# Kernel optimization log

Hardware: AMD Instinct MI355X
Metric: run time of the kernel (lower is better)

## Reference

```python
import jax, jax.numpy as jnp
import numpy as np

SEQ, B, E, H, V = 70, 128, 512, 1024, 10000


def setup_inputs() -> dict:
    key = jax.random.key(0)
    ks = jax.random.split(key, 24)
    u = lambda k, sh, a: jax.random.uniform(k, sh, jnp.float32, -a, a)
    kh = float(1.0 / np.sqrt(H))
    inp = {
        "inputs": jax.random.randint(ks[0], (SEQ, B), 0, V, dtype=jnp.int32),
        "hidden": jnp.zeros((2, B, H), jnp.float32),
        "emb_W": u(ks[1], (V, E), 0.1),
        "out_W": u(ks[2], (V, H), 0.1),
        "out_b": jnp.zeros((V,), jnp.float32),
    }
    i = 3
    for l, in_sz in enumerate([E, H]):
        for name, sh in [("Wir", (H, in_sz)), ("Wiz", (H, in_sz)), ("Wih", (H, in_sz)),
                         ("Whr", (H, H)), ("Whz", (H, H)), ("Whh", (H, H))]:
            inp[f"l{l}_{name}"] = u(ks[i], sh, kh); i += 1
        for name in ["bir", "biz", "bih"]:
            inp[f"l{l}_{name}"] = u(ks[i], (H,), kh); i += 1
    return inp


def gru_layer(xs, h0, Wir, bir, Whr, Wiz, biz, Whz, Wih, bih, Whh):
    # Precompute input-side projections for the whole sequence (big fused gemms).
    xr = jnp.einsum('sbe,he->sbh', xs, Wir) + bir  # (S,B,H)
    xz = jnp.einsum('sbe,he->sbh', xs, Wiz) + biz
    xh = jnp.einsum('sbe,he->sbh', xs, Wih) + bih

    def step(h, x_t):
        xr_t, xz_t, xh_t = x_t
        r = jax.nn.sigmoid(xr_t + h @ Whr.T)
        z = jax.nn.sigmoid(xz_t + h @ Whz.T)
        h1 = jnp.tanh(xh_t + r * (h @ Whh.T))
        h_new = (1.0 - z) * h1 + z * h
        return h_new, h_new

    hT, ys = jax.lax.scan(step, h0, (xr, xz, xh))
    return ys, hT


def reference(inputs, hidden, emb_W, out_W, out_b,
              l0_Wir, l0_Wiz, l0_Wih, l0_Whr, l0_Whz, l0_Whh, l0_bir, l0_biz, l0_bih,
              l1_Wir, l1_Wiz, l1_Wih, l1_Whr, l1_Whz, l1_Whh, l1_bir, l1_biz, l1_bih):
    emb = emb_W[inputs]  # (S,B,E)
    ys0, h0T = gru_layer(emb, hidden[0], l0_Wir, l0_bir, l0_Whr,
                         l0_Wiz, l0_biz, l0_Whz, l0_Wih, l0_bih, l0_Whh)
    ys1, h1T = gru_layer(ys0, hidden[1], l1_Wir, l1_bir, l1_Whr,
                         l1_Wiz, l1_biz, l1_Whz, l1_Wih, l1_bih, l1_Whh)
    logits = jnp.einsum('sbh,vh->sbv', ys1, out_W) + out_b  # (S,B,V)
    return logits, jnp.stack([h0T, h1T])
```

## Files before the change

kernel.cpp:

```cpp
#include <hip/hip_runtime.h>
#include <hip/hip_bf16.h>

#define SEQn 70
#define Bn 128
#define En 512
#define Hn 1024
#define Vn 10000
#define VPADn 10240
#define Mn (SEQn*Bn)
#define H3n (3*Hn)
#define BHn (Bn*Hn)
#define NBLK 192

typedef __hip_bfloat16 bf16;
typedef __attribute__((ext_vector_type(8))) short short8;
typedef __attribute__((ext_vector_type(4))) float f32x4;

__device__ __forceinline__ bf16 f2bf(float x){ return __float2bfloat16(x); }
__device__ __forceinline__ float bf2f(bf16 x){ return __bfloat162float(x); }

__device__ __forceinline__ void gl_lds16(const void* g, void* l){
  __builtin_amdgcn_global_load_lds((const __attribute__((address_space(1))) unsigned int*)g,
                                   (__attribute__((address_space(3))) unsigned int*)l, 16, 0, 0);
}


__global__ void cat3_w(const float* __restrict__ a, const float* __restrict__ b,
                       const float* __restrict__ c, bf16* __restrict__ d, int n){
  int i = blockIdx.x * 256 + threadIdx.x;
  if (i >= 3*n) return;
  const float* s = (i < n) ? a : ((i < 2*n) ? b : c);
  int off = (i < n) ? i : ((i < 2*n) ? i - n : i - 2*n);
  d[i] = f2bf(s[off]);
}

__global__ void cat3_f(const float* __restrict__ a, const float* __restrict__ b,
                       const float* __restrict__ c, float* __restrict__ d, int n){
  int i = blockIdx.x * 256 + threadIdx.x;
  if (i >= 3*n) return;
  d[i] = (i < n) ? a[i] : ((i < 2*n) ? b[i - n] : c[i - 2*n]);
}

__global__ void f2b_k(const float* __restrict__ s, bf16* __restrict__ d, int n){
  int i = blockIdx.x * 256 + threadIdx.x;
  if (i < n) d[i] = f2bf(s[i]);
}

__global__ void conv_outw(const float* __restrict__ s, bf16* __restrict__ d){
  long i = (long)blockIdx.x * 256 + threadIdx.x;
  if (i >= (long)VPADn * Hn) return;
  int row = (int)(i >> 10);
  d[i] = (row < Vn) ? f2bf(s[i]) : f2bf(0.f);
}

__global__ void embed_k(const int* __restrict__ idx, const float* __restrict__ eW,
                        bf16* __restrict__ out){
  const int sb = blockIdx.x;
  const int t = idx[sb];
  const float* s = eW + (long)t * En;
  bf16* d = out + (long)sb * En;
  for (int e = threadIdx.x; e < En; e += 256) d[e] = f2bf(s[e]);
}


template<bool OB, bool NB>
__global__ __launch_bounds__(256)
void gemm_bt(const bf16* __restrict__ A, const bf16* __restrict__ Bm,
             const float* __restrict__ bias, void* __restrict__ C,
             int K, int ldc, int nvalid)
{
  __shared__ __align__(16) bf16 As[128*64];
  __shared__ __align__(16) bf16 Bs[128*64];
  const int tid = threadIdx.x;
  const int l = tid & 63, w = tid >> 6;
  const int lr = l & 15, lk = l >> 4;
  const int wm = (w >> 1) * 64, wn = (w & 1) * 64;
  const int mt = blockIdx.y, nt = blockIdx.x;
  const bf16* Ag = A + (long)mt * 128 * K;
  const bf16* Bg = Bm + (long)nt * 128 * K;

  f32x4 acc[4][4] = {};

  for (int kb = 0; kb < K; kb += 64) {
#pragma unroll
    for (int r = 0; r < 4; ++r) {
      const int u = r * 256 + tid;
      const int row = u >> 3, kus = (u & 7) ^ (row & 7);
      gl_lds16(Ag + (long)row * K + kb + kus * 8, (char*)As + (r * 256 + w * 64) * 16);
    }
#pragma unroll
    for (int r = 0; r < 4; ++r) {
      const int u = r * 256 + tid;
      const int row = u >> 3, kus = (u & 7) ^ (row & 7);
      gl_lds16(Bg + (long)row * K + kb + kus * 8, (char*)Bs + (r * 256 + w * 64) * 16);
    }
    __syncthreads();
#pragma unroll
    for (int kh = 0; kh < 2; ++kh) {
      const int ku = kh * 4 + lk;
      short8 af[4], bfv[4];
#pragma unroll
      for (int i = 0; i < 4; ++i) {
        const int ar = wm + i * 16 + lr;
        af[i]  = *(const short8*)((const char*)As + ar * 128 + ((ku ^ (ar & 7)) * 16));
        const int br = wn + i * 16 + lr;
        bfv[i] = *(const short8*)((const char*)Bs + br * 128 + ((ku ^ (br & 7)) * 16));
      }
#pragma unroll
      for (int i = 0; i < 4; ++i)
#pragma unroll
        for (int j = 0; j < 4; ++j)
          acc[i][j] = __builtin_amdgcn_mfma_f32_16x16x32_bf16(af[i], bfv[j], acc[i][j], 0, 0, 0);
    }
    __syncthreads();
  }

#pragma unroll
  for (int i = 0; i < 4; ++i) {
#pragma unroll
    for (int j = 0; j < 4; ++j) {
      const int col = nt * 128 + wn + j * 16 + lr;
      const bool cok = (!NB) || (col < nvalid);
      const float bv = cok ? bias[col] : 0.f;
      const int row = mt * 128 + wm + i * 16 + lk * 4;
      if (cok) {
#pragma unroll
        for (int r = 0; r < 4; ++r) {
          const float v = acc[i][j][r] + bv;
          if (OB) ((bf16*)C)[(long)(row + r) * ldc + col] = f2bf(v);
          else    ((float*)C)[(long)(row + r) * ldc + col] = v;
        }
      }
    }
  }
}


#define LOADQ(buf, base)                                                     \
  _Pragma("unroll")                                                          \
  for (int q = 0; q < 8; ++q)                                                \
    buf[q] = *(const short8*)(Arow + ((base) + q) * 32 + lk * 8);

#define MFMAQ(buf, base)                                                     \
  _Pragma("unroll")                                                          \
  for (int q = 0; q < 8; ++q) {                                              \
    _Pragma("unroll")                                                        \
    for (int g = 0; g < 3; ++g) {                                            \
      const int brow = g * 16 + lr;                                          \
      const short8 bfrag = *(const short8*)(smem +                           \
          (size_t)(brow * 128 + ((((base) + q) * 4 + lk) ^ (brow & 7))) * 16); \
      acc[g] = __builtin_amdgcn_mfma_f32_16x16x32_bf16(buf[q], bfrag, acc[g], 0, 0, 0); \
    }                                                                        \
  }

__global__ __launch_bounds__(512, 2)
void gru_persist(const bf16* __restrict__ Wh0, const bf16* __restrict__ Wi1,
                 const bf16* __restrict__ Wh1, const float* __restrict__ b1,
                 const float* __restrict__ hidden, bf16* __restrict__ xg,
                 bf16* __restrict__ ys0, bf16* __restrict__ ys1,
                 float* __restrict__ hT, unsigned* __restrict__ bar)
{
  __shared__ __align__(16) char smem[98304];

  const int tid = threadIdx.x;
  const int lane = tid & 63, wid = tid >> 6;
  const int wbase = tid & ~63;
  const int lr = lane & 15, lk = lane >> 4;
  const int role = blockIdx.x >> 6, nb = blockIdx.x & 63;
  const int col0 = nb * 16;
  const int col = col0 + lr;

  unsigned myxcd;
  asm("s_getreg_b32 %0, hwreg(20, 0, 32)" : "=s"(myxcd));
  myxcd &= 7;
  unsigned* larrp  = bar + myxcd * 64;
  unsigned* gbarp  = bar + 512;
  unsigned* gflagp = bar + 544;

  const bf16* Wsrc = (role == 0) ? Wh0 : ((role == 1) ? Wi1 : Wh1);
#pragma unroll
  for (int it = 0; it < 12; ++it) {
    const int L = it * 512 + tid;
    const int row = L >> 7, up = L & 127, u = up ^ (row & 7);
    const int g3 = row >> 4, rr = row & 15;
    gl_lds16(Wsrc + ((size_t)(g3 * Hn + col0 + rr)) * Hn + (size_t)u * 8,
             smem + (it * 512 + wbase) * 16);
  }

  f32x4 hreg = {};
  float bv[3] = {};
  if (role != 1) {
    const float* hsrc = hidden + (role == 2 ? BHn : 0);
#pragma unroll
    for (int r = 0; r < 4; ++r)
      hreg[r] = hsrc[(size_t)(wid * 16 + lk * 4 + r) * Hn + col];
  } else {
#pragma unroll
    for (int g = 0; g < 3; ++g) bv[g] = b1[g * Hn + col];
  }
  asm volatile("s_waitcnt vmcnt(0)" ::: "memory");
  __syncthreads();

  unsigned perxcd = 0;
  if (tid == 0) {
    (void)__hip_atomic_fetch_add(larrp, 1u, __ATOMIC_RELAXED, __HIP_MEMORY_SCOPE_WORKGROUP);
    asm volatile("s_waitcnt vmcnt(0)" ::: "memory");
    unsigned g = __hip_atomic_fetch_add(gbarp, 1u, __ATOMIC_RELAXED, __HIP_MEMORY_SCOPE_AGENT);
    if (g == NBLK - 1)
      __hip_atomic_store(gflagp, 1u, __ATOMIC_RELAXED, __HIP_MEMORY_SCOPE_AGENT);
    while (__hip_atomic_load(gflagp, __ATOMIC_RELAXED, __HIP_MEMORY_SCOPE_AGENT) < 1u)
      __builtin_amdgcn_s_sleep(2);
    perxcd = __hip_atomic_fetch_add(larrp, 0u, __ATOMIC_RELAXED, __HIP_MEMORY_SCOPE_WORKGROUP);
  }
  __syncthreads();

  const int arow = wid * 16 + lr;

  for (int s = 0; s < 72; ++s) {
    const int t = s - role;
    if (t >= 0 && t < SEQn) {
      const bf16* Asrc = (role == 0) ? (ys0 + (size_t)t * BHn)
                       : (role == 1) ? (ys0 + (size_t)(t + 1) * BHn)
                                     : (ys1 + (size_t)t * BHn);
      const bf16* Arow = Asrc + (size_t)arow * Hn;
      f32x4 acc[3] = {};
      short8 aA[8], aB[8];
      unsigned short xus[12];
      LOADQ(aA, 0)
      LOADQ(aB, 8)
      if (role != 1) {
        const bf16* xsrc = xg + (size_t)t * Bn * (size_t)H3n;
#pragma unroll
        for (int g = 0; g < 3; ++g)
#pragma unroll
          for (int r = 0; r < 4; ++r) {
            const int row = wid * 16 + lk * 4 + r;
            const unsigned short* p =
                (const unsigned short*)(xsrc + (size_t)row * H3n + g * Hn + col);
            xus[g * 4 + r] = (role == 2)
              ? __hip_atomic_load((unsigned short*)p, __ATOMIC_RELAXED, __HIP_MEMORY_SCOPE_AGENT)
              : *p;
          }
      }
      MFMAQ(aA, 0)
      LOADQ(aA, 16)
      MFMAQ(aB, 8)
      LOADQ(aB, 24)
      MFMAQ(aA, 16)
      MFMAQ(aB, 24)

      if (role == 1) {
#pragma unroll
        for (int g = 0; g < 3; ++g)
#pragma unroll
          for (int r = 0; r < 4; ++r) {
            const int row = wid * 16 + lk * 4 + r;
            unsigned short v = __builtin_bit_cast(unsigned short, f2bf(acc[g][r] + bv[g]));
            __hip_atomic_store(
                (unsigned short*)&xg[((size_t)t * Bn + row) * H3n + g * Hn + col],
                v, __ATOMIC_RELAXED, __HIP_MEMORY_SCOPE_AGENT);
          }
      } else {
        bf16* ydst = ((role == 0) ? ys0 : ys1) + (size_t)(t + 1) * BHn;
#pragma unroll
        for (int r = 0; r < 4; ++r) {
          const int row = wid * 16 + lk * 4 + r;
          const float xr = bf2f(__builtin_bit_cast(bf16, xus[r]));
          const float xz = bf2f(__builtin_bit_cast(bf16, xus[4 + r]));
          const float xh = bf2f(__builtin_bit_cast(bf16, xus[8 + r]));
          const float rg = 1.f / (1.f + __expf(-(xr + acc[0][r])));
          const float zg = 1.f / (1.f + __expf(-(xz + acc[1][r])));
          const float hc = tanhf(xh + rg * acc[2][r]);
          const float hn = (1.f - zg) * hc + zg * hreg[r];
          hreg[r] = hn;
          unsigned short v = __builtin_bit_cast(unsigned short, f2bf(hn));
          __hip_atomic_store((unsigned short*)&ydst[(size_t)row * Hn + col],
                             v, __ATOMIC_RELAXED, __HIP_MEMORY_SCOPE_AGENT);
          if (t == SEQn - 1)
            hT[(role == 0 ? 0 : BHn) + (size_t)row * Hn + col] = hn;
        }
      }
    }
    if (s < 71) {
      __syncthreads();
      if (tid == 0) {
        unsigned a = __hip_atomic_fetch_add(larrp, 1u, __ATOMIC_RELAXED,
                                            __HIP_MEMORY_SCOPE_WORKGROUP);
        if (a == perxcd * (unsigned)(s + 2) - 1u) {
          unsigned g = __hip_atomic_fetch_add(gbarp, perxcd, __ATOMIC_RELAXED,
                                              __HIP_MEMORY_SCOPE_AGENT);
          if (g + perxcd == (unsigned)NBLK * (unsigned)(s + 2))
            __hip_atomic_store(gflagp, (unsigned)(s + 2), __ATOMIC_RELAXED,
                               __HIP_MEMORY_SCOPE_AGENT);
        }
        while (__hip_atomic_load(gflagp, __ATOMIC_RELAXED,
                                 __HIP_MEMORY_SCOPE_AGENT) < (unsigned)(s + 2))
          __builtin_amdgcn_s_sleep(2);
      }
      __syncthreads();
    }
  }
}


extern "C" void kernel_launch(void* const* d_in, const int* in_sizes, int n_in,
                              void* d_out, int out_size, void* d_ws, size_t ws_size,
                              hipStream_t stream)
{
  (void)in_sizes; (void)n_in; (void)out_size; (void)ws_size;
  const int*   inp    = (const int*)d_in[0];
  const float* hidden = (const float*)d_in[1];
  const float* embW   = (const float*)d_in[2];
  const float* outW   = (const float*)d_in[3];
  const float* outb   = (const float*)d_in[4];

  char* p = (char*)d_ws;
  auto take = [&](size_t n){ char* q = p; p += (n + 255) & ~(size_t)255; return q; };
  bf16*  l0Wi = (bf16*) take((size_t)H3n*En*2);
  bf16*  l0Wh = (bf16*) take((size_t)H3n*Hn*2);
  bf16*  l1Wi = (bf16*) take((size_t)H3n*Hn*2);
  bf16*  l1Wh = (bf16*) take((size_t)H3n*Hn*2);
  bf16*  oW   = (bf16*) take((size_t)VPADn*Hn*2);
  float* b0   = (float*)take((size_t)H3n*4);
  float* b1   = (float*)take((size_t)H3n*4);
  bf16*  emb  = (bf16*) take((size_t)Mn*En*2);
  bf16*  xg   = (bf16*) take((size_t)Mn*H3n*2);
  bf16*  ys0  = (bf16*) take((size_t)(SEQn+1)*BHn*2);
  bf16*  ys1  = (bf16*) take((size_t)(SEQn+1)*BHn*2);
  unsigned* bar = (unsigned*)take(4096);

  cat3_w<<<dim3((3*Hn*En+255)/256),256,0,stream>>>((const float*)d_in[5],(const float*)d_in[6],(const float*)d_in[7], l0Wi, Hn*En);
  cat3_w<<<dim3((3*Hn*Hn+255)/256),256,0,stream>>>((const float*)d_in[8],(const float*)d_in[9],(const float*)d_in[10], l0Wh, Hn*Hn);
  cat3_w<<<dim3((3*Hn*Hn+255)/256),256,0,stream>>>((const float*)d_in[14],(const float*)d_in[15],(const float*)d_in[16], l1Wi, Hn*Hn);
  cat3_w<<<dim3((3*Hn*Hn+255)/256),256,0,stream>>>((const float*)d_in[17],(const float*)d_in[18],(const float*)d_in[19], l1Wh, Hn*Hn);
  conv_outw<<<dim3((unsigned)(((long)VPADn*Hn+255)/256)),256,0,stream>>>(outW, oW);
  cat3_f<<<dim3((H3n+255)/256),256,0,stream>>>((const float*)d_in[11],(const float*)d_in[12],(const float*)d_in[13], b0, Hn);
  cat3_f<<<dim3((H3n+255)/256),256,0,stream>>>((const float*)d_in[20],(const float*)d_in[21],(const float*)d_in[22], b1, Hn);
  f2b_k<<<dim3((BHn+255)/256),256,0,stream>>>(hidden, ys0, BHn);
  f2b_k<<<dim3((BHn+255)/256),256,0,stream>>>(hidden + BHn, ys1, BHn);
  embed_k<<<dim3(Mn),256,0,stream>>>(inp, embW, emb);
  hipMemsetAsync(bar, 0, 4096, stream);

  gemm_bt<true,false><<<dim3(H3n/128, Mn/128),256,0,stream>>>(emb, l0Wi, b0, xg, En, H3n, H3n);

  float* hT = (float*)d_out + (size_t)SEQn * Bn * Vn;
  gru_persist<<<dim3(NBLK), 512, 0, stream>>>(l0Wh, l1Wi, l1Wh, b1, hidden,
                                              xg, ys0, ys1, hT, bar);

  gemm_bt<false,true><<<dim3(VPADn/128, Mn/128),256,0,stream>>>(ys1 + BHn, oW, outb, d_out, Hn, Vn, Vn);
}
```

Before: 1.113 ms.

## Halve persistent GRU block to 256 threads with two row tiles per wave

The persistent GRU kernel now runs 256 threads per block, and each wave handles two 16-row batch tiles instead of one. This lets every LDS weight fragment be reused across two MFMAs. The LDS weight layout changes to a lane-linear fragment order, which removes the XOR swizzle on reads. The K loop is double-buffered in groups of four k-chunks, with the B and A loads interleaved with the MFMAs. In exchange, each wave holds more registers and there are fewer waves to hide latency during the sequential per-step barrier chain.

```diff
diff --git a/kernel.cpp b/kernel.cpp
--- a/kernel.cpp
+++ b/kernel.cpp
@@ -136,24 +136,30 @@
 }
 
 
-#define LOADQ(buf, base)                                                     \
-  _Pragma("unroll")                                                          \
-  for (int q = 0; q < 8; ++q)                                                \
-    buf[q] = *(const short8*)(Arow + ((base) + q) * 32 + lk * 8);
-
-#define MFMAQ(buf, base)                                                     \
-  _Pragma("unroll")                                                          \
-  for (int q = 0; q < 8; ++q) {                                              \
-    _Pragma("unroll")                                                        \
-    for (int g = 0; g < 3; ++g) {                                            \
-      const int brow = g * 16 + lr;                                          \
-      const short8 bfrag = *(const short8*)(smem +                           \
-          (size_t)(brow * 128 + ((((base) + q) * 4 + lk) ^ (brow & 7))) * 16); \
-      acc[g] = __builtin_amdgcn_mfma_f32_16x16x32_bf16(buf[q], bfrag, acc[g], 0, 0, 0); \
-    }                                                                        \
-  }
-
-__global__ __launch_bounds__(512, 2)
+#define LDGRP(bb, aa, cbase)                                                   \
+  _Pragma("unroll")                                                            \
+  for (int g = 0; g < 3; ++g)                                                  \
+    _Pragma("unroll")                                                          \
+    for (int j = 0; j < 4; ++j)                                                \
+      bb[g][j] = *(const short8*)(smem +                                       \
+          ((size_t)((g * 32 + (cbase) + j) * 64 + lane)) * 16);                \
+  _Pragma("unroll")                                                            \
+  for (int rt = 0; rt < 2; ++rt)                                               \
+    _Pragma("unroll")                                                          \
+    for (int j = 0; j < 4; ++j)                                                \
+      aa[rt][j] = *(const short8*)(Arow[rt] + ((cbase) + j) * 32 + lk * 8);
+
+#define MFGRP(bb, aa)                                                          \
+  _Pragma("unroll")                                                            \
+  for (int j = 0; j < 4; ++j)                                                  \
+    _Pragma("unroll")                                                          \
+    for (int rt = 0; rt < 2; ++rt)                                             \
+      _Pragma("unroll")                                                        \
+      for (int g = 0; g < 3; ++g)                                              \
+        acc[rt][g] = __builtin_amdgcn_mfma_f32_16x16x32_bf16(                  \
+            aa[rt][j], bb[g][j], acc[rt][g], 0, 0, 0);
+
+__global__ __launch_bounds__(256, 1)
 void gru_persist(const bf16* __restrict__ Wh0, const bf16* __restrict__ Wi1,
                  const bf16* __restrict__ Wh1, const float* __restrict__ b1,
                  const float* __restrict__ hidden, bf16* __restrict__ xg,
@@ -179,21 +185,23 @@
 
   const bf16* Wsrc = (role == 0) ? Wh0 : ((role == 1) ? Wi1 : Wh1);
 #pragma unroll
-  for (int it = 0; it < 12; ++it) {
-    const int L = it * 512 + tid;
-    const int row = L >> 7, up = L & 127, u = up ^ (row & 7);
-    const int g3 = row >> 4, rr = row & 15;
-    gl_lds16(Wsrc + ((size_t)(g3 * Hn + col0 + rr)) * Hn + (size_t)u * 8,
-             smem + (it * 512 + wbase) * 16);
-  }
-
-  f32x4 hreg = {};
+  for (int it = 0; it < 24; ++it) {
+    const int u0 = it * 256 + wbase;
+    const int u  = u0 + lane;
+    const int g  = u >> 11, c = (u >> 6) & 31, l = u & 63;
+    gl_lds16(Wsrc + ((size_t)(g * Hn + col0 + (l & 15))) * Hn + c * 32 + (l >> 4) * 8,
+             smem + (size_t)u0 * 16);
+  }
+
+  f32x4 hreg[2] = {};
   float bv[3] = {};
   if (role != 1) {
     const float* hsrc = hidden + (role == 2 ? BHn : 0);
 #pragma unroll
-    for (int r = 0; r < 4; ++r)
-      hreg[r] = hsrc[(size_t)(wid * 16 + lk * 4 + r) * Hn + col];
+    for (int rt = 0; rt < 2; ++rt)
+#pragma unroll
+      for (int r = 0; r < 4; ++r)
+        hreg[rt][r] = hsrc[(size_t)((2 * wid + rt) * 16 + lk * 4 + r) * Hn + col];
   } else {
 #pragma unroll
     for (int g = 0; g < 3; ++g) bv[g] = b1[g * Hn + col];
@@ -214,71 +222,80 @@
   }
   __syncthreads();
 
-  const int arow = wid * 16 + lr;
-
   for (int s = 0; s < 72; ++s) {
     const int t = s - role;
     if (t >= 0 && t < SEQn) {
       const bf16* Asrc = (role == 0) ? (ys0 + (size_t)t * BHn)
                        : (role == 1) ? (ys0 + (size_t)(t + 1) * BHn)
                                      : (ys1 + (size_t)t * BHn);
-      const bf16* Arow = Asrc + (size_t)arow * Hn;
-      f32x4 acc[3] = {};
-      short8 aA[8], aB[8];
-      unsigned short xus[12];
-      LOADQ(aA, 0)
-      LOADQ(aB, 8)
+      const bf16* Arow[2];
+      Arow[0] = Asrc + (size_t)((2 * wid) * 16 + lr) * Hn;
+      Arow[1] = Asrc + (size_t)((2 * wid + 1) * 16 + lr) * Hn;
+      f32x4 acc[2][3] = {};
+      short8 bA[3][4], bB[3][4], aA[2][4], aB[2][4];
+      unsigned short xus[2][12];
+
+      LDGRP(bA, aA, 0)
+      LDGRP(bB, aB, 4)
       if (role != 1) {
         const bf16* xsrc = xg + (size_t)t * Bn * (size_t)H3n;
 #pragma unroll
-        for (int g = 0; g < 3; ++g)
-#pragma unroll
-          for (int r = 0; r < 4; ++r) {
-            const int row = wid * 16 + lk * 4 + r;
-            const unsigned short* p =
-                (const unsigned short*)(xsrc + (size_t)row * H3n + g * Hn + col);
-            xus[g * 4 + r] = (role == 2)
-              ? __hip_atomic_load((unsigned short*)p, __ATOMIC_RELAXED, __HIP_MEMORY_SCOPE_AGENT)
-              : *p;
-          }
-      }
-      MFMAQ(aA, 0)
-      LOADQ(aA, 16)
-      MFMAQ(aB, 8)
-      LOADQ(aB, 24)
-      MFMAQ(aA, 16)
-      MFMAQ(aB, 24)
+        for (int rt = 0; rt < 2; ++rt)
+#pragma unroll
+          for (int g = 0; g < 3; ++g)
+#pragma unroll
+            for (int r = 0; r < 4; ++r) {
+              const int row = (2 * wid + rt) * 16 + lk * 4 + r;
+              const unsigned short* p =
+                  (const unsigned short*)(xsrc + (size_t)row * H3n + g * Hn + col);
+              xus[rt][g * 4 + r] = (role == 2)
+                ? __hip_atomic_load((unsigned short*)p, __ATOMIC_RELAXED, __HIP_MEMORY_SCOPE_AGENT)
+                : *p;
+            }
+      }
+      MFGRP(bA, aA) LDGRP(bA, aA, 8)
+      MFGRP(bB, aB) LDGRP(bB, aB, 12)
+      MFGRP(bA, aA) LDGRP(bA, aA, 16)
+      MFGRP(bB, aB) LDGRP(bB, aB, 20)
+      MFGRP(bA, aA) LDGRP(bA, aA, 24)
+      MFGRP(bB, aB) LDGRP(bB, aB, 28)
+      MFGRP(bA, aA)
+      MFGRP(bB, aB)
 
       if (role == 1) {
 #pragma unroll
-        for (int g = 0; g < 3; ++g)
-#pragma unroll
-          for (int r = 0; r < 4; ++r) {
-            const int row = wid * 16 + lk * 4 + r;
-            unsigned short v = __builtin_bit_cast(unsigned short, f2bf(acc[g][r] + bv[g]));
-            __hip_atomic_store(
-                (unsigned short*)&xg[((size_t)t * Bn + row) * H3n + g * Hn + col],
-                v, __ATOMIC_RELAXED, __HIP_MEMORY_SCOPE_AGENT);
-          }
+        for (int rt = 0; rt < 2; ++rt)
+#pragma unroll
+          for (int g = 0; g < 3; ++g)
+#pragma unroll
+            for (int r = 0; r < 4; ++r) {
+              const int row = (2 * wid + rt) * 16 + lk * 4 + r;
+              unsigned short v = __builtin_bit_cast(unsigned short, f2bf(acc[rt][g][r] + bv[g]));
+              __hip_atomic_store(
+                  (unsigned short*)&xg[((size_t)t * Bn + row) * H3n + g * Hn + col],
+                  v, __ATOMIC_RELAXED, __HIP_MEMORY_SCOPE_AGENT);
+            }
       } else {
         bf16* ydst = ((role == 0) ? ys0 : ys1) + (size_t)(t + 1) * BHn;
 #pragma unroll
-        for (int r = 0; r < 4; ++r) {
-          const int row = wid * 16 + lk * 4 + r;
-          const float xr = bf2f(__builtin_bit_cast(bf16, xus[r]));
-          const float xz = bf2f(__builtin_bit_cast(bf16, xus[4 + r]));
-          const float xh = bf2f(__builtin_bit_cast(bf16, xus[8 + r]));
-          const float rg = 1.f / (1.f + __expf(-(xr + acc[0][r])));
-          const float zg = 1.f / (1.f + __expf(-(xz + acc[1][r])));
-          const float hc = tanhf(xh + rg * acc[2][r]);
-          const float hn = (1.f - zg) * hc + zg * hreg[r];
-          hreg[r] = hn;
-          unsigned short v = __builtin_bit_cast(unsigned short, f2bf(hn));
-          __hip_atomic_store((unsigned short*)&ydst[(size_t)row * Hn + col],
-                             v, __ATOMIC_RELAXED, __HIP_MEMORY_SCOPE_AGENT);
-          if (t == SEQn - 1)
-            hT[(role == 0 ? 0 : BHn) + (size_t)row * Hn + col] = hn;
-        }
+        for (int rt = 0; rt < 2; ++rt)
+#pragma unroll
+          for (int r = 0; r < 4; ++r) {
+            const int row = (2 * wid + rt) * 16 + lk * 4 + r;
+            const float xr = bf2f(__builtin_bit_cast(bf16, xus[rt][r]));
+            const float xz = bf2f(__builtin_bit_cast(bf16, xus[rt][4 + r]));
+            const float xh = bf2f(__builtin_bit_cast(bf16, xus[rt][8 + r]));
+            const float rg = 1.f / (1.f + __expf(-(xr + acc[rt][0][r])));
+            const float zg = 1.f / (1.f + __expf(-(xz + acc[rt][1][r])));
+            const float hc = tanhf(xh + rg * acc[rt][2][r]);
+            const float hn = (1.f - zg) * hc + zg * hreg[rt][r];
+            hreg[rt][r] = hn;
+            unsigned short v = __builtin_bit_cast(unsigned short, f2bf(hn));
+            __hip_atomic_store((unsigned short*)&ydst[(size_t)row * Hn + col],
+                               v, __ATOMIC_RELAXED, __HIP_MEMORY_SCOPE_AGENT);
+            if (t == SEQn - 1)
+              hT[(role == 0 ? 0 : BHn) + (size_t)row * Hn + col] = hn;
+          }
       }
     }
     if (s < 71) {
@@ -344,7 +361,7 @@
   gemm_bt<true,false><<<dim3(H3n/128, Mn/128),256,0,stream>>>(emb, l0Wi, b0, xg, En, H3n, H3n);
 
   float* hT = (float*)d_out + (size_t)SEQn * Bn * Vn;
-  gru_persist<<<dim3(NBLK), 512, 0, stream>>>(l0Wh, l1Wi, l1Wh, b1, hidden,
+  gru_persist<<<dim3(NBLK), 256, 0, stream>>>(l0Wh, l1Wi, l1Wh, b1, hidden,
                                               xg, ys0, ys1, hT, bar);
 
   gemm_bt<false,true><<<dim3(VPADn/128, Mn/128),256,0,stream>>>(ys1 + BHn, oW, outb, d_out, Hn, Vn, Vn);
```

Measured after the change: 1.133 ms. No clear change (+1.8%).
